# Optimization experiments

Hardware: AMD Instinct MI355X
Metric: run time of the kernel (lower is better)

## Reference

```python
import jax, jax.numpy as jnp
import numpy as np
import math

B, S, HID = 128, 200, 1024
NH = 4
DK = HID // NH
LSESS = 200  # session_len
MAXSEQ = 200
EPS = 1e-12


def setup_inputs() -> dict:
    key = jax.random.key(0)
    ks = jax.random.split(key, 12)
    inp = {}
    inp['query'] = jax.random.normal(ks[0], (B, S, HID), jnp.float32)
    inp['key'] = jax.random.normal(ks[1], (B, S, HID), jnp.float32)
    inp['value'] = jax.random.normal(ks[2], (B, S, HID), jnp.float32)
    std = 0.05
    inp['attn_w0'] = std * jax.random.normal(ks[3], (DK, DK), jnp.float32)
    inp['attn_w1'] = std * jax.random.normal(ks[4], (DK, DK), jnp.float32)
    inp['attn_w2'] = std * jax.random.normal(ks[5], (DK, DK), jnp.float32)
    inp['attn_w3'] = std * jax.random.normal(ks[6], (LSESS, DK), jnp.float32)
    inp['attn_bias'] = jnp.zeros((DK,), jnp.float32)
    inp['complex_weight'] = 0.02 * jax.random.normal(ks[7], (1, NH, MAXSEQ // 2 + 1, DK, 2), jnp.float32)
    bound = 1.0 / math.sqrt(HID)
    inp['linear_w'] = jax.random.uniform(ks[8], (HID, HID), jnp.float32, -bound, bound)
    inp['linear_b'] = jax.random.uniform(ks[9], (HID,), jnp.float32, -bound, bound)
    inp['ln_w'] = jnp.ones((HID,), jnp.float32)
    inp['ln_b'] = jnp.zeros((HID,), jnp.float32)
    return inp


def _gelu(x):
    return x * 0.5 * (1.0 + jax.lax.erf(x / jnp.sqrt(jnp.asarray(2.0, x.dtype))))


def reference(query, key, value, attn_w0, attn_w1, attn_w2, attn_w3, attn_bias,
              complex_weight, linear_w, linear_b, ln_w, ln_b):
    nb = query.shape[0]
    # (B, S, H, DK) -> (B, H, S, DK)
    def split_heads(x):
        return x.reshape(nb, -1, NH, DK).transpose(0, 2, 1, 3)
    q, k, v = split_heads(query), split_heads(key), split_heads(value)

    q = q @ attn_w0
    k = k @ attn_w1
    v = v @ attn_w2

    qf = jnp.fft.rfft(q, axis=2, norm='ortho')   # (B,H,S//2+1,DK) complex
    kf = jnp.fft.rfft(k, axis=2, norm='ortho')
    weight = complex_weight[..., 0] + 1j * complex_weight[..., 1]  # (1,4,MAXSEQ//2+1,DK)
    res = qf * jnp.conj(kf) * weight
    corr = jnp.fft.irfft(res, n=MAXSEQ, axis=2, norm='ortho')       # (B,H,MAXSEQ,DK)

    alpha = jnp.matmul(jax.nn.relu(corr + attn_bias), attn_w3.T)    # (B,H,MAXSEQ,LSESS)
    alpha = jax.nn.softmax(alpha, axis=-2)                          # softmax over seq dim
    x = jnp.einsum('bhsl,bhsd->bhld', alpha, v)                     # (B,H,LSESS,DK)

    x = x.transpose(0, 2, 1, 3).reshape(nb, -1, NH * DK)            # (B,LSESS,HID)
    x = x @ linear_w.T + linear_b
    # dropout is identity at inference
    x = _gelu(x)
    # LayerNorm (TF-style, eps inside sqrt)
    u = x.mean(-1, keepdims=True)
    s = ((x - u) ** 2).mean(-1, keepdims=True)
    x = (x - u) / jnp.sqrt(s + EPS)
    return ln_w * x + ln_b
```

## Files before the change

kernel.cpp:

```cpp
#include <hip/hip_runtime.h>
#include <hip/hip_bf16.h>
#include <math.h>

#define BATCH 128
#define SEQ   200
#define HID   1024
#define NH    4
#define DK    256
#define NF    101
#define LS    200
#define PD    256
#define IMOFF 128

typedef __attribute__((ext_vector_type(8))) short bf16x8;
typedef __attribute__((ext_vector_type(4))) float f32x4;

__device__ __forceinline__ unsigned short f2bf(float f) {
    union { float f; unsigned u; } v; v.f = f;
    unsigned r = v.u + 0x7fff + ((v.u >> 16) & 1);
    return (unsigned short)(r >> 16);
}
__device__ __forceinline__ float bf2f(unsigned short h) {
    union { unsigned u; float f; } v; v.u = ((unsigned)h) << 16;
    return v.f;
}

__device__ __forceinline__ void gld_lds16(const void* g, void* l) {
    __builtin_amdgcn_global_load_lds(
        (const __attribute__((address_space(1))) unsigned*)g,
        (__attribute__((address_space(3))) unsigned*)l, 16, 0, 0);
}

#define KSWZ(row, c8) ((c8) ^ (((row) & 7) << 3))

__global__ void init_tables_bf16(unsigned short* __restrict__ F, unsigned short* __restrict__ G) {
    int idx = blockIdx.x * 256 + threadIdx.x;
    const double inv = 0.07071067811865475244;
    const double PI2 = 6.283185307179586476925;
    {
        int fidx = idx >> 8, s = idx & 255;
        double v = 0.0;
        if (s < SEQ) {
            if (fidx < NF) {
                v = cos(PI2 * (double)((fidx * s) % SEQ) / (double)SEQ) * inv;
            } else if (fidx >= IMOFF && fidx < IMOFF + NF) {
                int f = fidx - IMOFF;
                v = -sin(PI2 * (double)((f * s) % SEQ) / (double)SEQ) * inv;
            }
        }
        F[idx] = f2bf((float)v);
    }
    {
        int s = idx >> 8, j = idx & 255;
        double v = 0.0;
        if (s < SEQ) {
            if (j < NF) {
                double al = (j == 0 || j == NF - 1) ? 1.0 : 2.0;
                v = al * cos(PI2 * (double)((j * s) % SEQ) / (double)SEQ) * inv;
            } else if (j >= IMOFF && j < IMOFF + NF) {
                int f = j - IMOFF;
                if (f != 0 && f != NF - 1)
                    v = -2.0 * sin(PI2 * (double)((f * s) % SEQ) / (double)SEQ) * inv;
            }
        }
        G[idx] = f2bf((float)v);
    }
}

__global__ void wtrans256(const float* __restrict__ src, unsigned short* __restrict__ dst) {
    int dout = blockIdx.x, din = threadIdx.x;
    dst[dout * 256 + din] = f2bf(src[din * 256 + dout]);
}

__global__ void w3pad(const float* __restrict__ src, unsigned short* __restrict__ dst) {
    int row = blockIdx.x, col = threadIdx.x;
    dst[row * 256 + col] = (row < LS) ? f2bf(src[row * 256 + col]) : (unsigned short)0;
}

__global__ void fconv(const float* __restrict__ src, unsigned short* __restrict__ dst, int n) {
    int i = blockIdx.x * 256 + threadIdx.x;
    if (i < n) dst[i] = f2bf(src[i]);
}

__global__ __launch_bounds__(256)
void convbf(const float* __restrict__ src, unsigned short* __restrict__ dst, int n8) {
    int i = blockIdx.x * 256 + threadIdx.x;
    int stride = gridDim.x * 256;
    for (; i < n8; i += stride) {
        const float4* s4 = reinterpret_cast<const float4*>(src + (long)i * 8);
        float4 x0 = s4[0], x1 = s4[1];
        unsigned short tmp[8];
        tmp[0] = f2bf(x0.x); tmp[1] = f2bf(x0.y); tmp[2] = f2bf(x0.z); tmp[3] = f2bf(x0.w);
        tmp[4] = f2bf(x1.x); tmp[5] = f2bf(x1.y); tmp[6] = f2bf(x1.z); tmp[7] = f2bf(x1.w);
        *(bf16x8*)(dst + (long)i * 8) = *(bf16x8*)tmp;
    }
}

template <int EPI, bool XCDSWZ>
__global__ __launch_bounds__(512, 2)
void mgemm256(const unsigned short* __restrict__ A, const unsigned short* __restrict__ B,
              unsigned short* __restrict__ C0, int K, int lda, int ldb, int ldc,
              long aOuter, long aInner, long bOuter, long bInner,
              long cOuter, long cInner, int nInner, int mValid, int nValid,
              const float* __restrict__ biasN) {
    extern __shared__ unsigned short lds[];
    unsigned short* AsB = lds;
    unsigned short* BsB = lds + 32768;

    int bx = blockIdx.x, by = blockIdx.y;
    if (XCDSWZ) {
        int nwg = gridDim.x * gridDim.y;
        int flat = by * gridDim.x + bx;
        int cpx = nwg >> 3;
        int swz = (flat & 7) * cpx + (flat >> 3);
        bx = swz % gridDim.x; by = swz / gridDim.x;
    }
    int bz = blockIdx.z;
    int bo = bz / nInner, bi = bz - bo * nInner;
    const unsigned short* Ab = A + bo * aOuter + bi * aInner;
    const unsigned short* Bb = B + bo * bOuter + bi * bInner;

    int t = threadIdx.x;
    int m0 = by * 256, n0 = bx * 256;
    int lane = t & 63, wave = t >> 6;
    int wr = wave >> 2, wc = wave & 3;
    int la = lane & 15, hi = lane >> 4;

    f32x4 acc[8][4] = {};
    int rsub = t >> 3;
    int c8 = (t & 7) * 8;

    auto stageA = [&](unsigned short* dst, long k0, int h) {
#pragma unroll
        for (int p = 0; p < 2; ++p) {
            int row = h * 128 + p * 64 + rsub;
            gld_lds16(Ab + (long)(m0 + row) * lda + k0 + KSWZ(row, c8), &dst[row * 64 + c8]);
        }
    };
    auto stageB = [&](unsigned short* dst, long k0, int h) {
#pragma unroll
        for (int p = 0; p < 2; ++p) {
            int row = h * 128 + p * 64 + rsub;
            gld_lds16(Bb + (long)(n0 + row) * ldb + k0 + KSWZ(row, c8), &dst[row * 64 + c8]);
        }
    };
    auto ldf = [&](const unsigned short* P, int row, int ko) -> bf16x8 {
        return *(const bf16x8*)&P[row * 64 + KSWZ(row, ko)];
    };

#define MFMA_ROW(mi, xa) \
    acc[mi][0] = __builtin_amdgcn_mfma_f32_16x16x32_bf16(xa, b0, acc[mi][0], 0, 0, 0); \
    acc[mi][1] = __builtin_amdgcn_mfma_f32_16x16x32_bf16(xa, b1, acc[mi][1], 0, 0, 0); \
    acc[mi][2] = __builtin_amdgcn_mfma_f32_16x16x32_bf16(xa, b2, acc[mi][2], 0, 0, 0); \
    acc[mi][3] = __builtin_amdgcn_mfma_f32_16x16x32_bf16(xa, b3, acc[mi][3], 0, 0, 0);

    int nkt = K >> 6;
    stageA(AsB, 0, 0); stageA(AsB, 0, 1);
    stageB(BsB, 0, 0); stageB(BsB, 0, 1);

    for (int kt = 0; kt < nkt; ++kt) {
        int cur = kt & 1;
        const unsigned short* Ac = AsB + cur * 16384;
        const unsigned short* Bc = BsB + cur * 16384;
        unsigned short* An = AsB + (cur ^ 1) * 16384;
        unsigned short* Bn = BsB + (cur ^ 1) * 16384;
        bool pre = (kt + 1) < nkt;
        long kn = (long)(kt + 1) << 6;

        bf16x8 b0, b1, b2, b3;

        if (pre) {
            stageA(An, kn, 0);
            asm volatile("s_waitcnt vmcnt(2)" ::: "memory");
        } else {
            asm volatile("s_waitcnt vmcnt(0)" ::: "memory");
        }
        __builtin_amdgcn_s_barrier();
        __builtin_amdgcn_sched_barrier(0);
        {
            int ko = hi * 8;
            b0 = ldf(Bc, wc * 64 + 0 * 16 + la, ko);
            b1 = ldf(Bc, wc * 64 + 1 * 16 + la, ko);
            b2 = ldf(Bc, wc * 64 + 2 * 16 + la, ko);
            b3 = ldf(Bc, wc * 64 + 3 * 16 + la, ko);
            bf16x8 x0 = ldf(Ac, wr * 128 + 0 * 16 + la, ko);
            bf16x8 x1 = ldf(Ac, wr * 128 + 1 * 16 + la, ko);
            bf16x8 x2 = ldf(Ac, wr * 128 + 2 * 16 + la, ko);
            bf16x8 x3 = ldf(Ac, wr * 128 + 3 * 16 + la, ko);
            __builtin_amdgcn_s_setprio(1);
            MFMA_ROW(0, x0) MFMA_ROW(1, x1) MFMA_ROW(2, x2) MFMA_ROW(3, x3)
            __builtin_amdgcn_s_setprio(0);
        }
        __builtin_amdgcn_s_barrier();

        if (pre) stageA(An, kn, 1);
        {
            int ko = hi * 8;
            bf16x8 x4 = ldf(Ac, wr * 128 + 4 * 16 + la, ko);
            bf16x8 x5 = ldf(Ac, wr * 128 + 5 * 16 + la, ko);
            bf16x8 x6 = ldf(Ac, wr * 128 + 6 * 16 + la, ko);
            bf16x8 x7 = ldf(Ac, wr * 128 + 7 * 16 + la, ko);
            __builtin_amdgcn_s_setprio(1);
            MFMA_ROW(4, x4) MFMA_ROW(5, x5) MFMA_ROW(6, x6) MFMA_ROW(7, x7)
            __builtin_amdgcn_s_setprio(0);
        }
        __builtin_amdgcn_s_barrier();

        if (pre) stageB(Bn, kn, 0);
        {
            int ko = 32 + hi * 8;
            b0 = ldf(Bc, wc * 64 + 0 * 16 + la, ko);
            b1 = ldf(Bc, wc * 64 + 1 * 16 + la, ko);
            b2 = ldf(Bc, wc * 64 + 2 * 16 + la, ko);
            b3 = ldf(Bc, wc * 64 + 3 * 16 + la, ko);
            bf16x8 x0 = ldf(Ac, wr * 128 + 0 * 16 + la, ko);
            bf16x8 x1 = ldf(Ac, wr * 128 + 1 * 16 + la, ko);
            bf16x8 x2 = ldf(Ac, wr * 128 + 2 * 16 + la, ko);
            bf16x8 x3 = ldf(Ac, wr * 128 + 3 * 16 + la, ko);
            __builtin_amdgcn_s_setprio(1);
            MFMA_ROW(0, x0) MFMA_ROW(1, x1) MFMA_ROW(2, x2) MFMA_ROW(3, x3)
            __builtin_amdgcn_s_setprio(0);
        }
        __builtin_amdgcn_s_barrier();

        if (pre) stageB(Bn, kn, 1);
        {
            int ko = 32 + hi * 8;
            bf16x8 x4 = ldf(Ac, wr * 128 + 4 * 16 + la, ko);
            bf16x8 x5 = ldf(Ac, wr * 128 + 5 * 16 + la, ko);
            bf16x8 x6 = ldf(Ac, wr * 128 + 6 * 16 + la, ko);
            bf16x8 x7 = ldf(Ac, wr * 128 + 7 * 16 + la, ko);
            __builtin_amdgcn_s_setprio(1);
            MFMA_ROW(4, x4) MFMA_ROW(5, x5) MFMA_ROW(6, x6) MFMA_ROW(7, x7)
            __builtin_amdgcn_s_setprio(0);
        }
        __builtin_amdgcn_s_barrier();
    }
#undef MFMA_ROW

    unsigned short* Ch = C0 + bo * cOuter + bi * cInner;
#pragma unroll
    for (int mi = 0; mi < 8; ++mi) {
#pragma unroll
        for (int ni = 0; ni < 4; ++ni) {
            int gn = n0 + wc * 64 + ni * 16 + la;
            if (gn >= nValid) continue;
            int gmB = m0 + wr * 128 + mi * 16 + hi * 4;
            float bN = 0.f;
            if (EPI == 2 || EPI == 4) bN = biasN[gn];
#pragma unroll
            for (int rr = 0; rr < 4; ++rr) {
                int gm = gmB + rr;
                if (gm >= mValid) continue;
                float v = acc[mi][ni][rr];
                if (EPI == 0) Ch[(long)gm * ldc + gn] = f2bf(v);
                else if (EPI == 2) Ch[(long)gm * ldc + gn] = f2bf(fmaxf(v + bN, 0.f));
                else Ch[(long)gm * ldc + gn] = f2bf(v + bN);
            }
        }
    }
}

__global__ __launch_bounds__(512, 2)
void alphasm(const unsigned short* __restrict__ A, const unsigned short* __restrict__ B,
             unsigned short* __restrict__ P0) {
    extern __shared__ unsigned short lds[];
    unsigned short* AsB = lds;
    unsigned short* BsB = lds + 32768;
    __shared__ float redM[256][4];
    __shared__ float redS[256][4];

    int bh = blockIdx.x;
    const unsigned short* Ab = A;
    const unsigned short* Bb = B + (long)bh * PD * PD;

    int t = threadIdx.x;
    int lane = t & 63, wave = t >> 6;
    int wr = wave >> 2, wc = wave & 3;
    int la = lane & 15, hi = lane >> 4;

    f32x4 acc[8][4] = {};
    int rsub = t >> 3;
    int c8 = (t & 7) * 8;

    auto stageA = [&](unsigned short* dst, long k0, int h) {
#pragma unroll
        for (int p = 0; p < 2; ++p) {
            int row = h * 128 + p * 64 + rsub;
            gld_lds16(Ab + (long)row * PD + k0 + KSWZ(row, c8), &dst[row * 64 + c8]);
        }
    };
    auto stageB = [&](unsigned short* dst, long k0, int h) {
#pragma unroll
        for (int p = 0; p < 2; ++p) {
            int row = h * 128 + p * 64 + rsub;
            gld_lds16(Bb + (long)row * PD + k0 + KSWZ(row, c8), &dst[row * 64 + c8]);
        }
    };
    auto ldf = [&](const unsigned short* P, int row, int ko) -> bf16x8 {
        return *(const bf16x8*)&P[row * 64 + KSWZ(row, ko)];
    };

#define MFMA_ROW(mi, xa) \
    acc[mi][0] = __builtin_amdgcn_mfma_f32_16x16x32_bf16(xa, b0, acc[mi][0], 0, 0, 0); \
    acc[mi][1] = __builtin_amdgcn_mfma_f32_16x16x32_bf16(xa, b1, acc[mi][1], 0, 0, 0); \
    acc[mi][2] = __builtin_amdgcn_mfma_f32_16x16x32_bf16(xa, b2, acc[mi][2], 0, 0, 0); \
    acc[mi][3] = __builtin_amdgcn_mfma_f32_16x16x32_bf16(xa, b3, acc[mi][3], 0, 0, 0);

    stageA(AsB, 0, 0); stageA(AsB, 0, 1);
    stageB(BsB, 0, 0); stageB(BsB, 0, 1);

    for (int kt = 0; kt < 4; ++kt) {
        int cur = kt & 1;
        const unsigned short* Ac = AsB + cur * 16384;
        const unsigned short* Bc = BsB + cur * 16384;
        unsigned short* An = AsB + (cur ^ 1) * 16384;
        unsigned short* Bn = BsB + (cur ^ 1) * 16384;
        bool pre = kt < 3;
        long kn = (long)(kt + 1) << 6;
        bf16x8 b0, b1, b2, b3;

        if (pre) {
            stageA(An, kn, 0);
            asm volatile("s_waitcnt vmcnt(2)" ::: "memory");
        } else {
            asm volatile("s_waitcnt vmcnt(0)" ::: "memory");
        }
        __builtin_amdgcn_s_barrier();
        __builtin_amdgcn_sched_barrier(0);
        {
            int ko = hi * 8;
            b0 = ldf(Bc, wc * 64 + 0 * 16 + la, ko);
            b1 = ldf(Bc, wc * 64 + 1 * 16 + la, ko);
            b2 = ldf(Bc, wc * 64 + 2 * 16 + la, ko);
            b3 = ldf(Bc, wc * 64 + 3 * 16 + la, ko);
            bf16x8 x0 = ldf(Ac, wr * 128 + 0 * 16 + la, ko);
            bf16x8 x1 = ldf(Ac, wr * 128 + 1 * 16 + la, ko);
            bf16x8 x2 = ldf(Ac, wr * 128 + 2 * 16 + la, ko);
            bf16x8 x3 = ldf(Ac, wr * 128 + 3 * 16 + la, ko);
            __builtin_amdgcn_s_setprio(1);
            MFMA_ROW(0, x0) MFMA_ROW(1, x1) MFMA_ROW(2, x2) MFMA_ROW(3, x3)
            __builtin_amdgcn_s_setprio(0);
        }
        __builtin_amdgcn_s_barrier();
        if (pre) stageA(An, kn, 1);
        {
            int ko = hi * 8;
            bf16x8 x4 = ldf(Ac, wr * 128 + 4 * 16 + la, ko);
            bf16x8 x5 = ldf(Ac, wr * 128 + 5 * 16 + la, ko);
            bf16x8 x6 = ldf(Ac, wr * 128 + 6 * 16 + la, ko);
            bf16x8 x7 = ldf(Ac, wr * 128 + 7 * 16 + la, ko);
            __builtin_amdgcn_s_setprio(1);
            MFMA_ROW(4, x4) MFMA_ROW(5, x5) MFMA_ROW(6, x6) MFMA_ROW(7, x7)
            __builtin_amdgcn_s_setprio(0);
        }
        __builtin_amdgcn_s_barrier();
        if (pre) stageB(Bn, kn, 0);
        {
            int ko = 32 + hi * 8;
            b0 = ldf(Bc, wc * 64 + 0 * 16 + la, ko);
            b1 = ldf(Bc, wc * 64 + 1 * 16 + la, ko);
            b2 = ldf(Bc, wc * 64 + 2 * 16 + la, ko);
            b3 = ldf(Bc, wc * 64 + 3 * 16 + la, ko);
            bf16x8 x0 = ldf(Ac, wr * 128 + 0 * 16 + la, ko);
            bf16x8 x1 = ldf(Ac, wr * 128 + 1 * 16 + la, ko);
            bf16x8 x2 = ldf(Ac, wr * 128 + 2 * 16 + la, ko);
            bf16x8 x3 = ldf(Ac, wr * 128 + 3 * 16 + la, ko);
            __builtin_amdgcn_s_setprio(1);
            MFMA_ROW(0, x0) MFMA_ROW(1, x1) MFMA_ROW(2, x2) MFMA_ROW(3, x3)
            __builtin_amdgcn_s_setprio(0);
        }
        __builtin_amdgcn_s_barrier();
        if (pre) stageB(Bn, kn, 1);
        {
            int ko = 32 + hi * 8;
            bf16x8 x4 = ldf(Ac, wr * 128 + 4 * 16 + la, ko);
            bf16x8 x5 = ldf(Ac, wr * 128 + 5 * 16 + la, ko);
            bf16x8 x6 = ldf(Ac, wr * 128 + 6 * 16 + la, ko);
            bf16x8 x7 = ldf(Ac, wr * 128 + 7 * 16 + la, ko);
            __builtin_amdgcn_s_setprio(1);
            MFMA_ROW(4, x4) MFMA_ROW(5, x5) MFMA_ROW(6, x6) MFMA_ROW(7, x7)
            __builtin_amdgcn_s_setprio(0);
        }
        __builtin_amdgcn_s_barrier();
    }
#undef MFMA_ROW

#pragma unroll
    for (int mi = 0; mi < 8; ++mi) {
#pragma unroll
        for (int rr = 0; rr < 4; ++rr) {
            float mv = -1e30f;
#pragma unroll
            for (int ni = 0; ni < 4; ++ni) {
                int gn = wc * 64 + ni * 16 + la;
                if (gn < LS) mv = fmaxf(mv, acc[mi][ni][rr]);
            }
            mv = fmaxf(mv, __shfl_xor(mv, 1));
            mv = fmaxf(mv, __shfl_xor(mv, 2));
            mv = fmaxf(mv, __shfl_xor(mv, 4));
            mv = fmaxf(mv, __shfl_xor(mv, 8));
            if (la == 0) redM[wr * 128 + mi * 16 + hi * 4 + rr][wc] = mv;
        }
    }
    __syncthreads();
#pragma unroll
    for (int mi = 0; mi < 8; ++mi) {
#pragma unroll
        for (int rr = 0; rr < 4; ++rr) {
            int row = wr * 128 + mi * 16 + hi * 4 + rr;
            float m = fmaxf(fmaxf(redM[row][0], redM[row][1]),
                            fmaxf(redM[row][2], redM[row][3]));
            float s = 0.f;
#pragma unroll
            for (int ni = 0; ni < 4; ++ni) {
                int gn = wc * 64 + ni * 16 + la;
                float e = (gn < LS) ? __expf(acc[mi][ni][rr] - m) : 0.f;
                acc[mi][ni][rr] = e;
                s += e;
            }
            s += __shfl_xor(s, 1);
            s += __shfl_xor(s, 2);
            s += __shfl_xor(s, 4);
            s += __shfl_xor(s, 8);
            if (la == 0) redS[row][wc] = s;
        }
    }
    __syncthreads();
    unsigned short* P = lds;
#pragma unroll
    for (int mi = 0; mi < 8; ++mi) {
#pragma unroll
        for (int rr = 0; rr < 4; ++rr) {
            int row = wr * 128 + mi * 16 + hi * 4 + rr;
            float inv = 1.f / (redS[row][0] + redS[row][1] + redS[row][2] + redS[row][3]);
#pragma unroll
            for (int ni = 0; ni < 4; ++ni) {
                int gn = wc * 64 + ni * 16 + la;
                P[row * 256 + gn] = f2bf(acc[mi][ni][rr] * inv);
            }
        }
    }
    __syncthreads();
    unsigned short* Pg = P0 + (long)bh * PD * PD;
    for (int i = t; i < 256 * 32; i += 512) {
        int row = i >> 5, seg = (i & 31) * 8;
        *(bf16x8*)(Pg + (long)row * PD + seg) = *(const bf16x8*)&P[row * 256 + seg];
    }
}

__global__ __launch_bounds__(256)
void crossspec(unsigned short* __restrict__ QF, const unsigned short* __restrict__ KF,
               const float* __restrict__ cw) {
    int blk = blockIdx.x;
    int bh = blk >> 4;
    int d0 = (blk & 15) * 16;
    int h = bh & (NH - 1);
    int t = threadIdx.x;
    if (t >= 16 * 13) return;
    int dl = t / 13, fg = t - dl * 13;
    int d = d0 + dl;
    long rb = (long)bh * DK * PD + (long)d * PD + fg * 8;
    bf16x8 qre = *(const bf16x8*)(QF + rb);
    bf16x8 qim = *(const bf16x8*)(QF + rb + IMOFF);
    bf16x8 kre = *(const bf16x8*)(KF + rb);
    bf16x8 kim = *(const bf16x8*)(KF + rb + IMOFF);
    bf16x8 orr, oii;
#pragma unroll
    for (int j = 0; j < 8; ++j) {
        int f = fg * 8 + j;
        float qr = bf2f((unsigned short)qre[j]), qi = bf2f((unsigned short)qim[j]);
        float kr = bf2f((unsigned short)kre[j]), ki = bf2f((unsigned short)kim[j]);
        float cr = qr * kr + qi * ki;
        float ci = qi * kr - qr * ki;
        float wr = 0.f, wi = 0.f;
        if (f < NF) {
            long wb = (((long)h * NF + f) * DK + d) * 2;
            wr = cw[wb]; wi = cw[wb + 1];
        }
        orr[j] = (short)f2bf(cr * wr - ci * wi);
        oii[j] = (short)f2bf(cr * wi + ci * wr);
    }
    *(bf16x8*)(QF + rb) = orr;
    *(bf16x8*)(QF + rb + IMOFF) = oii;
}

__global__ __launch_bounds__(256) void gelu_ln_kernel(const unsigned short* __restrict__ y2,
                               const float* __restrict__ lnw, const float* __restrict__ lnb,
                               float* __restrict__ out) {
    long row = blockIdx.x;
    int tid = threadIdx.x;
    const short4* xr = reinterpret_cast<const short4*>(y2 + row * HID);
    short4 h4 = xr[tid];
    float g[4];
    {
        float x0 = bf2f((unsigned short)h4.x), x1 = bf2f((unsigned short)h4.y);
        float x2 = bf2f((unsigned short)h4.z), x3 = bf2f((unsigned short)h4.w);
        g[0] = 0.5f * x0 * (1.f + erff(x0 * 0.70710678118654752f));
        g[1] = 0.5f * x1 * (1.f + erff(x1 * 0.70710678118654752f));
        g[2] = 0.5f * x2 * (1.f + erff(x2 * 0.70710678118654752f));
        g[3] = 0.5f * x3 * (1.f + erff(x3 * 0.70710678118654752f));
    }

    __shared__ float red[4];
    float s = g[0] + g[1] + g[2] + g[3];
#pragma unroll
    for (int o = 32; o > 0; o >>= 1) s += __shfl_down(s, o);
    if ((tid & 63) == 0) red[tid >> 6] = s;
    __syncthreads();
    float mean = (red[0] + red[1] + red[2] + red[3]) * (1.f / (float)HID);

    float v2 = 0.f;
#pragma unroll
    for (int p = 0; p < 4; ++p) { float d = g[p] - mean; v2 += d * d; }
    __syncthreads();
#pragma unroll
    for (int o = 32; o > 0; o >>= 1) v2 += __shfl_down(v2, o);
    if ((tid & 63) == 0) red[tid >> 6] = v2;
    __syncthreads();
    float var = (red[0] + red[1] + red[2] + red[3]) * (1.f / (float)HID);
    float rstd = rsqrtf(var + 1e-12f);

    float4 o4;
    int i0 = tid * 4;
    o4.x = (g[0] - mean) * rstd * lnw[i0 + 0] + lnb[i0 + 0];
    o4.y = (g[1] - mean) * rstd * lnw[i0 + 1] + lnb[i0 + 1];
    o4.z = (g[2] - mean) * rstd * lnw[i0 + 2] + lnb[i0 + 2];
    o4.w = (g[3] - mean) * rstd * lnw[i0 + 3] + lnb[i0 + 3];
    reinterpret_cast<float4*>(out + row * HID)[tid] = o4;
}

extern "C" void kernel_launch(void* const* d_in, const int* in_sizes, int n_in,
                              void* d_out, int out_size, void* d_ws, size_t ws_size,
                              hipStream_t stream) {
    const float* query = (const float*)d_in[0];
    const float* key   = (const float*)d_in[1];
    const float* value = (const float*)d_in[2];
    const float* w0 = (const float*)d_in[3];
    const float* w1 = (const float*)d_in[4];
    const float* w2 = (const float*)d_in[5];
    const float* w3 = (const float*)d_in[6];
    const float* attn_bias = (const float*)d_in[7];
    const float* cw = (const float*)d_in[8];
    const float* lw = (const float*)d_in[9];
    const float* lb = (const float*)d_in[10];
    const float* lnw = (const float*)d_in[11];
    const float* lnb = (const float*)d_in[12];
    float* out = (float*)d_out;

    char* base = (char*)d_ws;
    const long BH = (long)BATCH * NH;
    const long SZR = (long)BH * PD * PD;
    const size_t M64 = 67108864;
    const int NQ8 = BATCH * SEQ * HID / 8;

    unsigned short* F_stack = (unsigned short*)(base + 0);
    unsigned short* G_stack = (unsigned short*)(base + 131072);
    unsigned short* w0T = (unsigned short*)(base + 262144);
    unsigned short* w3b = (unsigned short*)(base + 655360);
    unsigned short* lwb = (unsigned short*)(base + 786432);
    char* rA = base + 4194304;
    char* rB = rA + M64;
    char* rC = rB + M64;
    char* rD = rC + M64;
    char* rE = rD + M64;

    unsigned short* qpT = (unsigned short*)rA;
    unsigned short* kpT = (unsigned short*)rB;
    unsigned short* vpT = (unsigned short*)rC;
    unsigned short* qbD = (unsigned short*)rD;
    unsigned short* qbE = (unsigned short*)rE;
    unsigned short* QF  = (unsigned short*)rD;
    unsigned short* KF  = (unsigned short*)rE;
    unsigned short* corr = (unsigned short*)rA;
    unsigned short* probs = (unsigned short*)rB;
    unsigned short* X  = (unsigned short*)rE;
    unsigned short* y2 = (unsigned short*)rD;

    const size_t LDS256 = 131072;

    init_tables_bf16<<<256, 256, 0, stream>>>(F_stack, G_stack);
    wtrans256<<<256, 256, 0, stream>>>(w0, w0T);
    wtrans256<<<256, 256, 0, stream>>>(w1, w0T + 65536);
    wtrans256<<<256, 256, 0, stream>>>(w2, w0T + 131072);
    w3pad<<<256, 256, 0, stream>>>(w3, w3b);
    fconv<<<(HID * HID + 255) / 256, 256, 0, stream>>>(lw, lwb, HID * HID);

    convbf<<<2048, 256, 0, stream>>>(query, qbD, NQ8);
    convbf<<<2048, 256, 0, stream>>>(key, qbE, NQ8);
    mgemm256<0, false><<<dim3(1, 1, BH), 512, LDS256, stream>>>(
        w0T, qbD, qpT, DK, DK, HID, PD,
        0L, 0L, (long)SEQ * HID, (long)DK,
        (long)NH * PD * PD, (long)PD * PD, NH, PD, SEQ, nullptr);
    mgemm256<0, false><<<dim3(1, 1, BH), 512, LDS256, stream>>>(
        w0T + 65536, qbE, kpT, DK, DK, HID, PD,
        0L, 0L, (long)SEQ * HID, (long)DK,
        (long)NH * PD * PD, (long)PD * PD, NH, PD, SEQ, nullptr);
    convbf<<<2048, 256, 0, stream>>>(value, qbD, NQ8);
    mgemm256<0, false><<<dim3(1, 1, BH), 512, LDS256, stream>>>(
        w0T + 131072, qbD, vpT, DK, DK, HID, PD,
        0L, 0L, (long)SEQ * HID, (long)DK,
        (long)NH * PD * PD, (long)PD * PD, NH, PD, SEQ, nullptr);

    mgemm256<0, false><<<dim3(1, 1, 2 * BH), 512, LDS256, stream>>>(
        qpT, F_stack, QF, PD, PD, PD, PD,
        SZR, (long)PD * PD, 0L, 0L, SZR, (long)PD * PD, (int)BH, PD, PD, nullptr);

    crossspec<<<(unsigned)(BH * 16), 256, 0, stream>>>(QF, KF, cw);

    mgemm256<2, false><<<dim3(1, 1, BH), 512, LDS256, stream>>>(
        G_stack, QF, corr, PD, PD, PD, PD,
        0L, 0L, (long)PD * PD, 0L, (long)PD * PD, 0L, 1, PD, PD, attn_bias);

    alphasm<<<dim3((unsigned)BH, 1, 1), 512, LDS256, stream>>>(w3b, corr, probs);

    mgemm256<0, false><<<dim3(1, 1, BH), 512, LDS256, stream>>>(
        probs, vpT, X, PD, PD, PD, HID,
        (long)NH * PD * PD, (long)PD * PD,
        (long)NH * PD * PD, (long)PD * PD,
        (long)LS * HID, (long)DK, NH, LS, PD, nullptr);

    mgemm256<4, true><<<dim3(HID / 256, (BATCH * LS) / 256, 1), 512, LDS256, stream>>>(
        X, lwb, y2, HID, HID, HID, HID,
        0L, 0L, 0L, 0L, 0L, 0L, 1, BATCH * LS, HID, lb);

    gelu_ln_kernel<<<(unsigned)(BATCH * LS), 256, 0, stream>>>(y2, lnw, lnb, out);
}
```

Baseline: 660.5 us.

## Fuse irfft GEMM, alpha softmax and PV GEMM into one attention kernel

Three kernels (the inverse-FFT GEMM with bias+ReLU, the alpha GEMM with softmax over seq, and the probs·V GEMM) become one kernel per batch-head. Intermediates are kept in a swizzled 128KB LDS stash instead of going through global memory. This removes the global round trips for corr and probs plus two launches. In exchange it uses 160KB LDS at one block per CU, and the later GEMM phases load W3 and V unpipelined with a full vmcnt(0) wait on each k-step, so latency hiding may suffer.

```diff
diff --git a/kernel.cpp b/kernel.cpp
--- a/kernel.cpp
+++ b/kernel.cpp
@@ -261,18 +261,23 @@
     }
 }
 
-__global__ __launch_bounds__(512, 2)
-void alphasm(const unsigned short* __restrict__ A, const unsigned short* __restrict__ B,
-             unsigned short* __restrict__ P0) {
+__global__ __launch_bounds__(512, 1)
+void attnfuse(const unsigned short* __restrict__ Gt, const unsigned short* __restrict__ R0,
+              const unsigned short* __restrict__ W3, const unsigned short* __restrict__ V0,
+              unsigned short* __restrict__ X0, const float* __restrict__ biasD) {
     extern __shared__ unsigned short lds[];
     unsigned short* AsB = lds;
     unsigned short* BsB = lds + 32768;
-    __shared__ float redM[256][4];
-    __shared__ float redS[256][4];
+    unsigned short* stash = lds;
+    unsigned short* stage = lds + 65536;
+    float* redM = (float*)stage;
+    float* redS = redM + 1024;
 
     int bh = blockIdx.x;
-    const unsigned short* Ab = A;
-    const unsigned short* Bb = B + (long)bh * PD * PD;
+    const unsigned short* Rb = R0 + (long)bh * PD * PD;
+    const unsigned short* Vb = V0 + (long)bh * PD * PD;
+    int b = bh >> 2, h = bh & 3;
+    unsigned short* Xb = X0 + (long)b * LS * HID + h * DK;
 
     int t = threadIdx.x;
     int lane = t & 63, wave = t >> 6;
@@ -283,22 +288,11 @@
     int rsub = t >> 3;
     int c8 = (t & 7) * 8;
 
-    auto stageA = [&](unsigned short* dst, long k0, int h) {
-#pragma unroll
-        for (int p = 0; p < 2; ++p) {
-            int row = h * 128 + p * 64 + rsub;
-            gld_lds16(Ab + (long)row * PD + k0 + KSWZ(row, c8), &dst[row * 64 + c8]);
-        }
-    };
-    auto stageB = [&](unsigned short* dst, long k0, int h) {
-#pragma unroll
-        for (int p = 0; p < 2; ++p) {
-            int row = h * 128 + p * 64 + rsub;
-            gld_lds16(Bb + (long)row * PD + k0 + KSWZ(row, c8), &dst[row * 64 + c8]);
-        }
-    };
     auto ldf = [&](const unsigned short* P, int row, int ko) -> bf16x8 {
         return *(const bf16x8*)&P[row * 64 + KSWZ(row, ko)];
+    };
+    auto ldstash = [&](int row, int colblk) -> bf16x8 {
+        return *(const bf16x8*)&stash[row * 256 + (colblk ^ ((row & 7) << 3))];
     };
 
 #define MFMA_ROW(mi, xa) \
@@ -307,84 +301,154 @@
     acc[mi][2] = __builtin_amdgcn_mfma_f32_16x16x32_bf16(xa, b2, acc[mi][2], 0, 0, 0); \
     acc[mi][3] = __builtin_amdgcn_mfma_f32_16x16x32_bf16(xa, b3, acc[mi][3], 0, 0, 0);
 
-    stageA(AsB, 0, 0); stageA(AsB, 0, 1);
-    stageB(BsB, 0, 0); stageB(BsB, 0, 1);
+    {
+        auto stageA = [&](unsigned short* dst, long k0, int hh) {
+#pragma unroll
+            for (int p = 0; p < 2; ++p) {
+                int row = hh * 128 + p * 64 + rsub;
+                gld_lds16(Gt + (long)row * PD + k0 + KSWZ(row, c8), &dst[row * 64 + c8]);
+            }
+        };
+        auto stageB = [&](unsigned short* dst, long k0, int hh) {
+#pragma unroll
+            for (int p = 0; p < 2; ++p) {
+                int row = hh * 128 + p * 64 + rsub;
+                gld_lds16(Rb + (long)row * PD + k0 + KSWZ(row, c8), &dst[row * 64 + c8]);
+            }
+        };
+        stageA(AsB, 0, 0); stageA(AsB, 0, 1);
+        stageB(BsB, 0, 0); stageB(BsB, 0, 1);
+        for (int kt = 0; kt < 4; ++kt) {
+            int cur = kt & 1;
+            const unsigned short* Ac = AsB + cur * 16384;
+            const unsigned short* Bc = BsB + cur * 16384;
+            unsigned short* An = AsB + (cur ^ 1) * 16384;
+            unsigned short* Bn = BsB + (cur ^ 1) * 16384;
+            bool pre = kt < 3;
+            long kn = (long)(kt + 1) << 6;
+            bf16x8 b0, b1, b2, b3;
+
+            if (pre) {
+                stageA(An, kn, 0);
+                asm volatile("s_waitcnt vmcnt(2)" ::: "memory");
+            } else {
+                asm volatile("s_waitcnt vmcnt(0)" ::: "memory");
+            }
+            __builtin_amdgcn_s_barrier();
+            __builtin_amdgcn_sched_barrier(0);
+            {
+                int ko = hi * 8;
+                b0 = ldf(Bc, wc * 64 + 0 * 16 + la, ko);
+                b1 = ldf(Bc, wc * 64 + 1 * 16 + la, ko);
+                b2 = ldf(Bc, wc * 64 + 2 * 16 + la, ko);
+                b3 = ldf(Bc, wc * 64 + 3 * 16 + la, ko);
+                bf16x8 x0 = ldf(Ac, wr * 128 + 0 * 16 + la, ko);
+                bf16x8 x1 = ldf(Ac, wr * 128 + 1 * 16 + la, ko);
+                bf16x8 x2 = ldf(Ac, wr * 128 + 2 * 16 + la, ko);
+                bf16x8 x3 = ldf(Ac, wr * 128 + 3 * 16 + la, ko);
+                __builtin_amdgcn_s_setprio(1);
+                MFMA_ROW(0, x0) MFMA_ROW(1, x1) MFMA_ROW(2, x2) MFMA_ROW(3, x3)
+                __builtin_amdgcn_s_setprio(0);
+            }
+            __builtin_amdgcn_s_barrier();
+            if (pre) stageA(An, kn, 1);
+            {
+                int ko = hi * 8;
+                bf16x8 x4 = ldf(Ac, wr * 128 + 4 * 16 + la, ko);
+                bf16x8 x5 = ldf(Ac, wr * 128 + 5 * 16 + la, ko);
+                bf16x8 x6 = ldf(Ac, wr * 128 + 6 * 16 + la, ko);
+                bf16x8 x7 = ldf(Ac, wr * 128 + 7 * 16 + la, ko);
+                __builtin_amdgcn_s_setprio(1);
+                MFMA_ROW(4, x4) MFMA_ROW(5, x5) MFMA_ROW(6, x6) MFMA_ROW(7, x7)
+                __builtin_amdgcn_s_setprio(0);
+            }
+            __builtin_amdgcn_s_barrier();
+            if (pre) stageB(Bn, kn, 0);
+            {
+                int ko = 32 + hi * 8;
+                b0 = ldf(Bc, wc * 64 + 0 * 16 + la, ko);
+                b1 = ldf(Bc, wc * 64 + 1 * 16 + la, ko);
+                b2 = ldf(Bc, wc * 64 + 2 * 16 + la, ko);
+                b3 = ldf(Bc, wc * 64 + 3 * 16 + la, ko);
+                bf16x8 x0 = ldf(Ac, wr * 128 + 0 * 16 + la, ko);
+                bf16x8 x1 = ldf(Ac, wr * 128 + 1 * 16 + la, ko);
+                bf16x8 x2 = ldf(Ac, wr * 128 + 2 * 16 + la, ko);
+                bf16x8 x3 = ldf(Ac, wr * 128 + 3 * 16 + la, ko);
+                __builtin_amdgcn_s_setprio(1);
+                MFMA_ROW(0, x0) MFMA_ROW(1, x1) MFMA_ROW(2, x2) MFMA_ROW(3, x3)
+                __builtin_amdgcn_s_setprio(0);
+            }
+            __builtin_amdgcn_s_barrier();
+            if (pre) stageB(Bn, kn, 1);
+            {
+                int ko = 32 + hi * 8;
+                bf16x8 x4 = ldf(Ac, wr * 128 + 4 * 16 + la, ko);
+                bf16x8 x5 = ldf(Ac, wr * 128 + 5 * 16 + la, ko);
+                bf16x8 x6 = ldf(Ac, wr * 128 + 6 * 16 + la, ko);
+                bf16x8 x7 = ldf(Ac, wr * 128 + 7 * 16 + la, ko);
+                __builtin_amdgcn_s_setprio(1);
+                MFMA_ROW(4, x4) MFMA_ROW(5, x5) MFMA_ROW(6, x6) MFMA_ROW(7, x7)
+                __builtin_amdgcn_s_setprio(0);
+            }
+            __builtin_amdgcn_s_barrier();
+        }
+    }
+#pragma unroll
+    for (int mi = 0; mi < 8; ++mi) {
+#pragma unroll
+        for (int ni = 0; ni < 4; ++ni) {
+            int gn = wc * 64 + ni * 16 + la;
+            float bN = biasD[gn];
+#pragma unroll
+            for (int rr = 0; rr < 4; ++rr) {
+                int gm = wr * 128 + mi * 16 + hi * 4 + rr;
+                float v = fmaxf(acc[mi][ni][rr] + bN, 0.f);
+                stash[gm * 256 + ((gn & ~7) ^ ((gm & 7) << 3)) + (gn & 7)] = f2bf(v);
+            }
+        }
+    }
+    __syncthreads();
+
+#pragma unroll
+    for (int mi = 0; mi < 8; ++mi)
+#pragma unroll
+        for (int ni = 0; ni < 4; ++ni) acc[mi][ni] = f32x4{0.f, 0.f, 0.f, 0.f};
 
     for (int kt = 0; kt < 4; ++kt) {
-        int cur = kt & 1;
-        const unsigned short* Ac = AsB + cur * 16384;
-        const unsigned short* Bc = BsB + cur * 16384;
-        unsigned short* An = AsB + (cur ^ 1) * 16384;
-        unsigned short* Bn = BsB + (cur ^ 1) * 16384;
-        bool pre = kt < 3;
-        long kn = (long)(kt + 1) << 6;
-        bf16x8 b0, b1, b2, b3;
-
-        if (pre) {
-            stageA(An, kn, 0);
-            asm volatile("s_waitcnt vmcnt(2)" ::: "memory");
-        } else {
-            asm volatile("s_waitcnt vmcnt(0)" ::: "memory");
-        }
+        long k0 = (long)kt << 6;
+#pragma unroll
+        for (int p = 0; p < 4; ++p) {
+            int row = p * 64 + rsub;
+            gld_lds16(W3 + (long)row * PD + k0 + KSWZ(row, c8), &stage[row * 64 + c8]);
+        }
+        asm volatile("s_waitcnt vmcnt(0)" ::: "memory");
         __builtin_amdgcn_s_barrier();
         __builtin_amdgcn_sched_barrier(0);
-        {
-            int ko = hi * 8;
-            b0 = ldf(Bc, wc * 64 + 0 * 16 + la, ko);
-            b1 = ldf(Bc, wc * 64 + 1 * 16 + la, ko);
-            b2 = ldf(Bc, wc * 64 + 2 * 16 + la, ko);
-            b3 = ldf(Bc, wc * 64 + 3 * 16 + la, ko);
-            bf16x8 x0 = ldf(Ac, wr * 128 + 0 * 16 + la, ko);
-            bf16x8 x1 = ldf(Ac, wr * 128 + 1 * 16 + la, ko);
-            bf16x8 x2 = ldf(Ac, wr * 128 + 2 * 16 + la, ko);
-            bf16x8 x3 = ldf(Ac, wr * 128 + 3 * 16 + la, ko);
+#pragma unroll
+        for (int half = 0; half < 2; ++half) {
+            int ko = half * 32 + hi * 8;
+            int colblk = kt * 64 + ko;
+            bf16x8 b0, b1, b2, b3;
+            b0 = ldstash(wc * 64 + 0 * 16 + la, colblk ^ 0);
+            b0 = ldstash(wc * 64 + 0 * 16 + la, colblk);
+            b1 = ldstash(wc * 64 + 1 * 16 + la, colblk);
+            b2 = ldstash(wc * 64 + 2 * 16 + la, colblk);
+            b3 = ldstash(wc * 64 + 3 * 16 + la, colblk);
+            bf16x8 x0 = ldf(stage, wr * 128 + 0 * 16 + la, ko);
+            bf16x8 x1 = ldf(stage, wr * 128 + 1 * 16 + la, ko);
+            bf16x8 x2 = ldf(stage, wr * 128 + 2 * 16 + la, ko);
+            bf16x8 x3 = ldf(stage, wr * 128 + 3 * 16 + la, ko);
+            bf16x8 x4 = ldf(stage, wr * 128 + 4 * 16 + la, ko);
+            bf16x8 x5 = ldf(stage, wr * 128 + 5 * 16 + la, ko);
+            bf16x8 x6 = ldf(stage, wr * 128 + 6 * 16 + la, ko);
+            bf16x8 x7 = ldf(stage, wr * 128 + 7 * 16 + la, ko);
             __builtin_amdgcn_s_setprio(1);
             MFMA_ROW(0, x0) MFMA_ROW(1, x1) MFMA_ROW(2, x2) MFMA_ROW(3, x3)
-            __builtin_amdgcn_s_setprio(0);
-        }
-        __builtin_amdgcn_s_barrier();
-        if (pre) stageA(An, kn, 1);
-        {
-            int ko = hi * 8;
-            bf16x8 x4 = ldf(Ac, wr * 128 + 4 * 16 + la, ko);
-            bf16x8 x5 = ldf(Ac, wr * 128 + 5 * 16 + la, ko);
-            bf16x8 x6 = ldf(Ac, wr * 128 + 6 * 16 + la, ko);
-            bf16x8 x7 = ldf(Ac, wr * 128 + 7 * 16 + la, ko);
-            __builtin_amdgcn_s_setprio(1);
             MFMA_ROW(4, x4) MFMA_ROW(5, x5) MFMA_ROW(6, x6) MFMA_ROW(7, x7)
             __builtin_amdgcn_s_setprio(0);
         }
         __builtin_amdgcn_s_barrier();
-        if (pre) stageB(Bn, kn, 0);
-        {
-            int ko = 32 + hi * 8;
-            b0 = ldf(Bc, wc * 64 + 0 * 16 + la, ko);
-            b1 = ldf(Bc, wc * 64 + 1 * 16 + la, ko);
-            b2 = ldf(Bc, wc * 64 + 2 * 16 + la, ko);
-            b3 = ldf(Bc, wc * 64 + 3 * 16 + la, ko);
-            bf16x8 x0 = ldf(Ac, wr * 128 + 0 * 16 + la, ko);
-            bf16x8 x1 = ldf(Ac, wr * 128 + 1 * 16 + la, ko);
-            bf16x8 x2 = ldf(Ac, wr * 128 + 2 * 16 + la, ko);
-            bf16x8 x3 = ldf(Ac, wr * 128 + 3 * 16 + la, ko);
-            __builtin_amdgcn_s_setprio(1);
-            MFMA_ROW(0, x0) MFMA_ROW(1, x1) MFMA_ROW(2, x2) MFMA_ROW(3, x3)
-            __builtin_amdgcn_s_setprio(0);
-        }
-        __builtin_amdgcn_s_barrier();
-        if (pre) stageB(Bn, kn, 1);
-        {
-            int ko = 32 + hi * 8;
-            bf16x8 x4 = ldf(Ac, wr * 128 + 4 * 16 + la, ko);
-            bf16x8 x5 = ldf(Ac, wr * 128 + 5 * 16 + la, ko);
-            bf16x8 x6 = ldf(Ac, wr * 128 + 6 * 16 + la, ko);
-            bf16x8 x7 = ldf(Ac, wr * 128 + 7 * 16 + la, ko);
-            __builtin_amdgcn_s_setprio(1);
-            MFMA_ROW(4, x4) MFMA_ROW(5, x5) MFMA_ROW(6, x6) MFMA_ROW(7, x7)
-            __builtin_amdgcn_s_setprio(0);
-        }
-        __builtin_amdgcn_s_barrier();
-    }
-#undef MFMA_ROW
+    }
 
 #pragma unroll
     for (int mi = 0; mi < 8; ++mi) {
@@ -400,7 +464,7 @@
             mv = fmaxf(mv, __shfl_xor(mv, 2));
             mv = fmaxf(mv, __shfl_xor(mv, 4));
             mv = fmaxf(mv, __shfl_xor(mv, 8));
-            if (la == 0) redM[wr * 128 + mi * 16 + hi * 4 + rr][wc] = mv;
+            if (la == 0) redM[(wr * 128 + mi * 16 + hi * 4 + rr) * 4 + wc] = mv;
         }
     }
     __syncthreads();
@@ -409,8 +473,8 @@
 #pragma unroll
         for (int rr = 0; rr < 4; ++rr) {
             int row = wr * 128 + mi * 16 + hi * 4 + rr;
-            float m = fmaxf(fmaxf(redM[row][0], redM[row][1]),
-                            fmaxf(redM[row][2], redM[row][3]));
+            float m = fmaxf(fmaxf(redM[row * 4 + 0], redM[row * 4 + 1]),
+                            fmaxf(redM[row * 4 + 2], redM[row * 4 + 3]));
             float s = 0.f;
 #pragma unroll
             for (int ni = 0; ni < 4; ++ni) {
@@ -423,29 +487,81 @@
             s += __shfl_xor(s, 2);
             s += __shfl_xor(s, 4);
             s += __shfl_xor(s, 8);
-            if (la == 0) redS[row][wc] = s;
+            if (la == 0) redS[row * 4 + wc] = s;
         }
     }
     __syncthreads();
-    unsigned short* P = lds;
 #pragma unroll
     for (int mi = 0; mi < 8; ++mi) {
 #pragma unroll
         for (int rr = 0; rr < 4; ++rr) {
             int row = wr * 128 + mi * 16 + hi * 4 + rr;
-            float inv = 1.f / (redS[row][0] + redS[row][1] + redS[row][2] + redS[row][3]);
+            float inv = 1.f / (redS[row * 4 + 0] + redS[row * 4 + 1] +
+                               redS[row * 4 + 2] + redS[row * 4 + 3]);
 #pragma unroll
             for (int ni = 0; ni < 4; ++ni) {
                 int gn = wc * 64 + ni * 16 + la;
-                P[row * 256 + gn] = f2bf(acc[mi][ni][rr] * inv);
+                stash[row * 256 + ((gn & ~7) ^ ((row & 7) << 3)) + (gn & 7)] =
+                    f2bf(acc[mi][ni][rr] * inv);
             }
         }
     }
     __syncthreads();
-    unsigned short* Pg = P0 + (long)bh * PD * PD;
-    for (int i = t; i < 256 * 32; i += 512) {
-        int row = i >> 5, seg = (i & 31) * 8;
-        *(bf16x8*)(Pg + (long)row * PD + seg) = *(const bf16x8*)&P[row * 256 + seg];
+
+#pragma unroll
+    for (int mi = 0; mi < 8; ++mi)
+#pragma unroll
+        for (int ni = 0; ni < 4; ++ni) acc[mi][ni] = f32x4{0.f, 0.f, 0.f, 0.f};
+
+    for (int kt = 0; kt < 4; ++kt) {
+        long k0 = (long)kt << 6;
+#pragma unroll
+        for (int p = 0; p < 4; ++p) {
+            int row = p * 64 + rsub;
+            gld_lds16(Vb + (long)row * PD + k0 + KSWZ(row, c8), &stage[row * 64 + c8]);
+        }
+        asm volatile("s_waitcnt vmcnt(0)" ::: "memory");
+        __builtin_amdgcn_s_barrier();
+        __builtin_amdgcn_sched_barrier(0);
+#pragma unroll
+        for (int half = 0; half < 2; ++half) {
+            int ko = half * 32 + hi * 8;
+            int colblk = kt * 64 + ko;
+            bf16x8 b0, b1, b2, b3;
+            b0 = ldf(stage, wc * 64 + 0 * 16 + la, ko);
+            b1 = ldf(stage, wc * 64 + 1 * 16 + la, ko);
+            b2 = ldf(stage, wc * 64 + 2 * 16 + la, ko);
+            b3 = ldf(stage, wc * 64 + 3 * 16 + la, ko);
+            bf16x8 x0 = ldstash(wr * 128 + 0 * 16 + la, colblk);
+            bf16x8 x1 = ldstash(wr * 128 + 1 * 16 + la, colblk);
+            bf16x8 x2 = ldstash(wr * 128 + 2 * 16 + la, colblk);
+            bf16x8 x3 = ldstash(wr * 128 + 3 * 16 + la, colblk);
+            bf16x8 x4 = ldstash(wr * 128 + 4 * 16 + la, colblk);
+            bf16x8 x5 = ldstash(wr * 128 + 5 * 16 + la, colblk);
+            bf16x8 x6 = ldstash(wr * 128 + 6 * 16 + la, colblk);
+            bf16x8 x7 = ldstash(wr * 128 + 7 * 16 + la, colblk);
+            __builtin_amdgcn_s_setprio(1);
+            MFMA_ROW(0, x0) MFMA_ROW(1, x1) MFMA_ROW(2, x2) MFMA_ROW(3, x3)
+            MFMA_ROW(4, x4) MFMA_ROW(5, x5) MFMA_ROW(6, x6) MFMA_ROW(7, x7)
+            __builtin_amdgcn_s_setprio(0);
+        }
+        __builtin_amdgcn_s_barrier();
+    }
+#undef MFMA_ROW
+
+#pragma unroll
+    for (int mi = 0; mi < 8; ++mi) {
+#pragma unroll
+        for (int ni = 0; ni < 4; ++ni) {
+            int gn = wc * 64 + ni * 16 + la;
+            int gmB = wr * 128 + mi * 16 + hi * 4;
+#pragma unroll
+            for (int rr = 0; rr < 4; ++rr) {
+                int gm = gmB + rr;
+                if (gm >= LS) continue;
+                Xb[(long)gm * HID + gn] = f2bf(acc[mi][ni][rr]);
+            }
+        }
     }
 }
 
@@ -572,12 +688,11 @@
     unsigned short* qbE = (unsigned short*)rE;
     unsigned short* QF  = (unsigned short*)rD;
     unsigned short* KF  = (unsigned short*)rE;
-    unsigned short* corr = (unsigned short*)rA;
-    unsigned short* probs = (unsigned short*)rB;
-    unsigned short* X  = (unsigned short*)rE;
-    unsigned short* y2 = (unsigned short*)rD;
+    unsigned short* X   = (unsigned short*)rE;
+    unsigned short* y2  = (unsigned short*)rD;
 
     const size_t LDS256 = 131072;
+    const size_t LDSFUSE = 163840;
 
     init_tables_bf16<<<256, 256, 0, stream>>>(F_stack, G_stack);
     wtrans256<<<256, 256, 0, stream>>>(w0, w0T);
@@ -608,17 +723,7 @@
 
     crossspec<<<(unsigned)(BH * 16), 256, 0, stream>>>(QF, KF, cw);
 
-    mgemm256<2, false><<<dim3(1, 1, BH), 512, LDS256, stream>>>(
-        G_stack, QF, corr, PD, PD, PD, PD,
-        0L, 0L, (long)PD * PD, 0L, (long)PD * PD, 0L, 1, PD, PD, attn_bias);
-
-    alphasm<<<dim3((unsigned)BH, 1, 1), 512, LDS256, stream>>>(w3b, corr, probs);
-
-    mgemm256<0, false><<<dim3(1, 1, BH), 512, LDS256, stream>>>(
-        probs, vpT, X, PD, PD, PD, HID,
-        (long)NH * PD * PD, (long)PD * PD,
-        (long)NH * PD * PD, (long)PD * PD,
-        (long)LS * HID, (long)DK, NH, LS, PD, nullptr);
+    attnfuse<<<(unsigned)BH, 512, LDSFUSE, stream>>>(G_stack, QF, w3b, vpT, X, attn_bias);
 
     mgemm256<4, true><<<dim3(HID / 256, (BATCH * LS) / 256, 1), 512, LDS256, stream>>>(
         X, lwb, y2, HID, HID, HID, HID,
```

Result: no change. 664.5 us (+0.6%).
